# Kernel optimization log

Hardware: AMD Instinct MI355X
Metric: run time of the kernel (lower is better)

## Reference

```python
import jax, jax.numpy as jnp
import numpy as np
import math

B, T, E, HS = 8, 2048, 1024, 64  # batch, seq, n_embd, head_size (n_embd // n_head)


def setup_inputs() -> dict:
    key = jax.random.key(0)
    ks = jax.random.split(key, 7)
    sc = 1.0 / math.sqrt(E)  # roughly nn.Linear init scale
    return {
        "inputs": jax.random.normal(ks[0], (B, T, E), dtype=jnp.float32),
        "Wq": jax.random.normal(ks[1], (HS, E), dtype=jnp.float32) * sc,
        "bq": jax.random.normal(ks[2], (HS,), dtype=jnp.float32) * sc,
        "Wk": jax.random.normal(ks[3], (HS, E), dtype=jnp.float32) * sc,
        "bk": jax.random.normal(ks[4], (HS,), dtype=jnp.float32) * sc,
        "Wv": jax.random.normal(ks[5], (HS, E), dtype=jnp.float32) * sc,
        "bv": jax.random.normal(ks[6], (HS,), dtype=jnp.float32) * sc,
    }


def reference(inputs, Wq, bq, Wk, bk, Wv, bv):
    # Linear projections: x @ W.T + b  -> [B, T, HS]
    q = jnp.einsum("bte,he->bth", inputs, Wq) + bq
    k = jnp.einsum("bte,he->bth", inputs, Wk) + bk
    v = jnp.einsum("bte,he->bth", inputs, Wv) + bv

    # Scaled scores: [B, T, T]
    scores = jnp.einsum("bqh,bkh->bqk", q, k) / math.sqrt(HS)

    # Causal mask exactly as original: scores * tril - 1e12 * (1 - tril)
    tril = jnp.tril(jnp.ones((T, T), dtype=scores.dtype))
    scores = scores * tril - 1e12 * (1.0 - tril)

    attn = jax.nn.softmax(scores, axis=-1)
    # dropout p=0 (eval) -> identity
    out = jnp.einsum("bqk,bkh->bqh", attn, v)  # [B, T, HS]
    return out
```

## Files before the change

kernel.cpp:

```cpp
#include <hip/hip_runtime.h>
#include <hip/hip_bf16.h>


typedef __attribute__((ext_vector_type(8))) short short8;
typedef __attribute__((ext_vector_type(4))) float f32x4;

#if __has_builtin(__builtin_amdgcn_exp2f)
#define EXP2(x) __builtin_amdgcn_exp2f(x)
#else
#define EXP2(x) exp2f(x)
#endif

#define QSCALE 0.18033688f

__device__ inline unsigned short f2bf(float f) {
    unsigned int u = __builtin_bit_cast(unsigned int, f);
    u += 0x7FFF + ((u >> 16) & 1);
    return (unsigned short)(u >> 16);
}

__global__ __launch_bounds__(64) void prep_w(
    const float* __restrict__ Wq, const float* __restrict__ Wk,
    const float* __restrict__ Wv, unsigned short* __restrict__ Wfrag)
{
    const int ct = blockIdx.x >> 5;
    const int kk = blockIdx.x & 31;
    const int L  = threadIdx.x;
    const int l16 = L & 15, quad = L >> 4;
    const int col = ct * 16 + l16;

    const float* W; int row; float scale = 1.0f;
    if (col < 64)       { W = Wq; row = col;       scale = QSCALE; }
    else if (col < 128) { W = Wk; row = col - 64; }
    else                { W = Wv; row = col - 128; }

    const float* p = W + (size_t)row * 1024 + kk * 32 + quad * 8;
    alignas(16) unsigned short tmp[8];
    #pragma unroll
    for (int j = 0; j < 8; j++) tmp[j] = f2bf(p[j] * scale);
    unsigned short* dst = Wfrag + ((size_t)blockIdx.x * 64 + L) * 8;
    *reinterpret_cast<int4*>(dst) = *reinterpret_cast<const int4*>(tmp);
}

#define XLD 1032
__global__ __launch_bounds__(256, 4) void qkv_kernel(
    const float* __restrict__ x, const unsigned short* __restrict__ Wfrag,
    const float* __restrict__ bq, const float* __restrict__ bk,
    const float* __restrict__ bv,
    unsigned short* __restrict__ Qb, unsigned short* __restrict__ Kf,
    unsigned short* __restrict__ Vf)
{
    __shared__ alignas(16) unsigned short xs[32][XLD];

    const int tid  = threadIdx.x;
    const int m0   = blockIdx.x * 32;
    const int lane = tid & 63;
    const int w    = tid >> 6;
    const int l16  = lane & 15, quad = lane >> 4;

    #pragma unroll
    for (int i = 0; i < 16; i++) {
        int ch  = tid + 256 * i;
        int r   = ch >> 7;
        int c16 = ch & 127;
        const float* p = x + (size_t)(m0 + r) * 1024 + c16 * 8;
        float4 v0 = *reinterpret_cast<const float4*>(p);
        float4 v1 = *reinterpret_cast<const float4*>(p + 4);
        alignas(16) unsigned short t8[8] = {
            f2bf(v0.x), f2bf(v0.y), f2bf(v0.z), f2bf(v0.w),
            f2bf(v1.x), f2bf(v1.y), f2bf(v1.z), f2bf(v1.w)};
        *reinterpret_cast<int4*>(&xs[r][c16 * 8]) =
            *reinterpret_cast<const int4*>(t8);
    }
    __syncthreads();

    const int ct0 = w * 3;
    f32x4 acc[2][3];
    #pragma unroll
    for (int a = 0; a < 2; a++)
        #pragma unroll
        for (int c = 0; c < 3; c++) acc[a][c] = (f32x4){0.f, 0.f, 0.f, 0.f};

    short8 bcur[3];
    #pragma unroll
    for (int ci = 0; ci < 3; ci++)
        bcur[ci] = *reinterpret_cast<const short8*>(
            Wfrag + ((size_t)((ct0 + ci) * 32) * 64 + lane) * 8);

    for (int kk = 0; kk < 32; kk++) {
        const int kkn = (kk < 31) ? kk + 1 : 31;
        short8 bnxt[3];
        #pragma unroll
        for (int ci = 0; ci < 3; ci++)
            bnxt[ci] = *reinterpret_cast<const short8*>(
                Wfrag + ((size_t)((ct0 + ci) * 32 + kkn) * 64 + lane) * 8);

        short8 a0 = *reinterpret_cast<const short8*>(&xs[l16][kk * 32 + quad * 8]);
        short8 a1 = *reinterpret_cast<const short8*>(&xs[16 + l16][kk * 32 + quad * 8]);
        #pragma unroll
        for (int ci = 0; ci < 3; ci++) {
            acc[0][ci] = __builtin_amdgcn_mfma_f32_16x16x32_bf16(a0, bcur[ci], acc[0][ci], 0, 0, 0);
            acc[1][ci] = __builtin_amdgcn_mfma_f32_16x16x32_bf16(a1, bcur[ci], acc[1][ci], 0, 0, 0);
        }
        #pragma unroll
        for (int ci = 0; ci < 3; ci++) bcur[ci] = bnxt[ci];
    }

    const int bi = m0 >> 11;
    #pragma unroll
    for (int rt = 0; rt < 2; rt++) {
        #pragma unroll
        for (int ci = 0; ci < 3; ci++) {
            const int ct = ct0 + ci;
            const int h  = (ct & 3) * 16 + l16;
            if (ct < 4) {
                float bias = bq[h] * QSCALE;
                #pragma unroll
                for (int i = 0; i < 4; i++) {
                    size_t m = (size_t)(m0 + rt * 16 + quad * 4 + i);
                    Qb[m * 64 + h] = f2bf(acc[rt][ci][i] + bias);
                }
            } else if (ct < 8) {
                float bias = bk[h];
                #pragma unroll
                for (int i = 0; i < 4; i++) {
                    int t   = m0 + rt * 16 + quad * 4 + i;
                    int tin = t & 63;
                    int kt  = (t & 2047) >> 6;
                    int f   = ((h >> 5) << 2) | (tin >> 4);
                    int lp  = (tin & 15) | (((h >> 3) & 3) << 4);
                    Kf[(((size_t)(bi * 32 + kt) * 8 + f) * 64 + lp) * 8 + (h & 7)]
                        = f2bf(acc[rt][ci][i] + bias);
                }
            } else {
                float bias = bv[h];
                int tb  = m0 + rt * 16 + quad * 4;
                int tin = tb & 63;
                int kt  = (tb & 2047) >> 6;
                int f   = ((tin >> 5) << 2) | (h >> 4);
                int lp  = (h & 15) | (((tin >> 3) & 3) << 4);
                alignas(8) unsigned short tmp[4];
                #pragma unroll
                for (int i = 0; i < 4; i++) tmp[i] = f2bf(acc[rt][ci][i] + bias);
                unsigned short* dst =
                    Vf + (((size_t)(bi * 32 + kt) * 8 + f) * 64 + lp) * 8 + (tin & 7);
                *reinterpret_cast<int2*>(dst) = *reinterpret_cast<const int2*>(tmp);
            }
        }
    }
}

__global__ __launch_bounds__(256, 3) void attn_part(
    const unsigned short* __restrict__ Qb,
    const unsigned short* __restrict__ Kf,
    const unsigned short* __restrict__ Vf,
    float* __restrict__ Opart, float* __restrict__ Lpart)
{
    __shared__ alignas(16) unsigned short ps[4][16][72];

    const int bid = blockIdx.x;
    const int b   = bid & 7;
    const int j64 = (bid >> 3) & 31;
    const int c   = bid >> 8;
    const int nkt = j64 + 1;
    const int kt0 = c * 8;
    if (kt0 >= nkt) return;
    const int kt1 = (kt0 + 8 < nkt) ? kt0 + 8 : nkt;

    const int tid  = threadIdx.x;
    const int w    = tid >> 6;
    const int lane = tid & 63;
    const int l16  = lane & 15, quad = lane >> 4;
    const int j16  = j64 * 4 + w;
    const int q0   = j16 * 16;

    const unsigned short* qrow = Qb + ((size_t)(b * 2048 + q0 + l16)) * 64 + quad * 8;
    short8 aq0 = *reinterpret_cast<const short8*>(qrow);
    short8 aq1 = *reinterpret_cast<const short8*>(qrow + 32);

    const unsigned short* Kbat = Kf + (size_t)(b * 32) * 4096;
    const unsigned short* Vbat = Vf + (size_t)(b * 32) * 4096;

    f32x4 o[4];
    float rs[4] = {0.f, 0.f, 0.f, 0.f};
    #pragma unroll
    for (int i = 0; i < 4; i++) o[i] = (f32x4){0, 0, 0, 0};

    short8 kfr[8];
    {
        const unsigned short* kb = Kbat + (size_t)kt0 * 4096 + lane * 8;
        #pragma unroll
        for (int f = 0; f < 8; f++)
            kfr[f] = *reinterpret_cast<const short8*>(kb + f * 512);
    }

    for (int kt = kt0; kt < kt1; kt++) {
        const int ktn = (kt + 1 < kt1) ? kt + 1 : kt;
        short8 kn[8];
        {
            const unsigned short* kb = Kbat + (size_t)ktn * 4096 + lane * 8;
            #pragma unroll
            for (int f = 0; f < 8; f++)
                kn[f] = *reinterpret_cast<const short8*>(kb + f * 512);
        }
        short8 vfr[8];
        {
            const unsigned short* vb = Vbat + (size_t)kt * 4096 + lane * 8;
            #pragma unroll
            for (int f = 0; f < 8; f++)
                vfr[f] = *reinterpret_cast<const short8*>(vb + f * 512);
        }

        f32x4 s[4];
        #pragma unroll
        for (int ct = 0; ct < 4; ct++) s[ct] = (f32x4){0, 0, 0, 0};
        #pragma unroll
        for (int ks2 = 0; ks2 < 2; ks2++) {
            short8 aqf = ks2 ? aq1 : aq0;
            #pragma unroll
            for (int ct = 0; ct < 4; ct++)
                s[ct] = __builtin_amdgcn_mfma_f32_16x16x32_bf16(
                    aqf, kfr[ks2 * 4 + ct], s[ct], 0, 0, 0);
        }

        if (kt == nkt - 1) {
            #pragma unroll
            for (int ct = 0; ct < 4; ct++) {
                int col = kt * 64 + ct * 16 + l16;
                #pragma unroll
                for (int i = 0; i < 4; i++) {
                    int row = q0 + quad * 4 + i;
                    if (col > row) s[ct][i] = -1e30f;
                }
            }
        }

        #pragma unroll
        for (int ct = 0; ct < 4; ct++) {
            #pragma unroll
            for (int i = 0; i < 4; i++) {
                float p = EXP2(s[ct][i]);
                rs[i] += p;
                ps[w][quad * 4 + i][ct * 16 + l16] = f2bf(p);
            }
        }

        short8 ap0 = *reinterpret_cast<const short8*>(&ps[w][l16][quad * 8]);
        short8 ap1 = *reinterpret_cast<const short8*>(&ps[w][l16][32 + quad * 8]);

        #pragma unroll
        for (int ks2 = 0; ks2 < 2; ks2++) {
            short8 apf = ks2 ? ap1 : ap0;
            #pragma unroll
            for (int ct = 0; ct < 4; ct++)
                o[ct] = __builtin_amdgcn_mfma_f32_16x16x32_bf16(
                    apf, vfr[ks2 * 4 + ct], o[ct], 0, 0, 0);
        }

        #pragma unroll
        for (int f = 0; f < 8; f++) kfr[f] = kn[f];
    }

    const int pid = (c << 10) | (j16 << 3) | b;
    float* op = Opart + (size_t)pid * 1024;
    #pragma unroll
    for (int i = 0; i < 4; i++) {
        int r = quad * 4 + i;
        #pragma unroll
        for (int ct = 0; ct < 4; ct++)
            op[(size_t)r * 64 + ct * 16 + l16] = o[ct][i];
        float v = rs[i];
        v += __shfl_xor(v, 1);
        v += __shfl_xor(v, 2);
        v += __shfl_xor(v, 4);
        v += __shfl_xor(v, 8);
        if (l16 == 0) Lpart[(size_t)pid * 16 + r] = v;
    }
}

__global__ __launch_bounds__(256) void attn_combine(
    const float* __restrict__ Opart, const float* __restrict__ Lpart,
    float* __restrict__ out)
{
    const int t0 = blockIdx.x * 256 + threadIdx.x;
    #pragma unroll
    for (int it = 0; it < 2; it++) {
        const int v    = t0 + it * 131072;
        const int flat = v * 4;
        const int b    = flat >> 17;
        const int rem  = flat & 131071;
        const int t    = rem >> 6;
        const int h0   = rem & 63;
        const int j16  = t >> 4, row = t & 15;
        const int nch  = ((j16 >> 2) + 8) >> 3;
        const int pidb = (j16 << 3) | b;

        float4 acc = {0.f, 0.f, 0.f, 0.f};
        float  l   = 0.f;
        for (int c = 0; c < nch; c++) {
            const int pid = (c << 10) | pidb;
            const float* op = Opart + (size_t)pid * 1024 + row * 64 + h0;
            float4 x4 = *reinterpret_cast<const float4*>(op);
            acc.x += x4.x; acc.y += x4.y; acc.z += x4.z; acc.w += x4.w;
            l += Lpart[(size_t)pid * 16 + row];
        }
        const float inv = 1.f / l;
        float4 r = {acc.x * inv, acc.y * inv, acc.z * inv, acc.w * inv};
        *reinterpret_cast<float4*>(out + flat) = r;
    }
}

extern "C" void kernel_launch(void* const* d_in, const int* in_sizes, int n_in,
                              void* d_out, int out_size, void* d_ws, size_t ws_size,
                              hipStream_t stream) {
    const float* x  = (const float*)d_in[0];
    const float* Wq = (const float*)d_in[1];
    const float* bq = (const float*)d_in[2];
    const float* Wk = (const float*)d_in[3];
    const float* bk = (const float*)d_in[4];
    const float* Wv = (const float*)d_in[5];
    const float* bv = (const float*)d_in[6];
    float* out = (float*)d_out;

    unsigned short* Qb    = (unsigned short*)d_ws;
    unsigned short* Kf    = Qb + (size_t)16384 * 64;
    unsigned short* Vf    = Kf + (size_t)16384 * 64;
    unsigned short* Wfrag = Vf + (size_t)16384 * 64;
    float* Opart = (float*)(Wfrag + (size_t)12 * 32 * 64 * 8);
    float* Lpart = Opart + (size_t)4096 * 1024;

    prep_w<<<384, 64, 0, stream>>>(Wq, Wk, Wv, Wfrag);
    qkv_kernel<<<512, 256, 0, stream>>>(x, Wfrag, bq, bk, bv, Qb, Kf, Vf);
    attn_part<<<1024, 256, 0, stream>>>(Qb, Kf, Vf, Opart, Lpart);
    attn_combine<<<512, 256, 0, stream>>>(Opart, Lpart, out);
}
```

Before: 138.7 us.

## Halve attention KV chunk size, transpose score MFMA, drop K prefetch

```diff
diff --git a/kernel.cpp b/kernel.cpp
--- a/kernel.cpp
+++ b/kernel.cpp
@@ -150,7 +150,7 @@
     }
 }
 
-__global__ __launch_bounds__(256, 3) void attn_part(
+__global__ __launch_bounds__(256, 4) void attn_part(
     const unsigned short* __restrict__ Qb,
     const unsigned short* __restrict__ Kf,
     const unsigned short* __restrict__ Vf,
@@ -163,9 +163,9 @@
     const int j64 = (bid >> 3) & 31;
     const int c   = bid >> 8;
     const int nkt = j64 + 1;
-    const int kt0 = c * 8;
+    const int kt0 = c * 4;
     if (kt0 >= nkt) return;
-    const int kt1 = (kt0 + 8 < nkt) ? kt0 + 8 : nkt;
+    const int kt1 = (kt0 + 4 < nkt) ? kt0 + 4 : nkt;
 
     const int tid  = threadIdx.x;
     const int w    = tid >> 6;
@@ -182,33 +182,20 @@
     const unsigned short* Vbat = Vf + (size_t)(b * 32) * 4096;
 
     f32x4 o[4];
-    float rs[4] = {0.f, 0.f, 0.f, 0.f};
+    float rs = 0.f;
     #pragma unroll
     for (int i = 0; i < 4; i++) o[i] = (f32x4){0, 0, 0, 0};
 
-    short8 kfr[8];
-    {
-        const unsigned short* kb = Kbat + (size_t)kt0 * 4096 + lane * 8;
-        #pragma unroll
-        for (int f = 0; f < 8; f++)
-            kfr[f] = *reinterpret_cast<const short8*>(kb + f * 512);
-    }
-
     for (int kt = kt0; kt < kt1; kt++) {
-        const int ktn = (kt + 1 < kt1) ? kt + 1 : kt;
-        short8 kn[8];
+        short8 kfr[8], vfr[8];
         {
-            const unsigned short* kb = Kbat + (size_t)ktn * 4096 + lane * 8;
-            #pragma unroll
-            for (int f = 0; f < 8; f++)
-                kn[f] = *reinterpret_cast<const short8*>(kb + f * 512);
-        }
-        short8 vfr[8];
-        {
+            const unsigned short* kb = Kbat + (size_t)kt * 4096 + lane * 8;
             const unsigned short* vb = Vbat + (size_t)kt * 4096 + lane * 8;
             #pragma unroll
-            for (int f = 0; f < 8; f++)
+            for (int f = 0; f < 8; f++) {
+                kfr[f] = *reinterpret_cast<const short8*>(kb + f * 512);
                 vfr[f] = *reinterpret_cast<const short8*>(vb + f * 512);
+            }
         }
 
         f32x4 s[4];
@@ -220,29 +207,32 @@
             #pragma unroll
             for (int ct = 0; ct < 4; ct++)
                 s[ct] = __builtin_amdgcn_mfma_f32_16x16x32_bf16(
-                    aqf, kfr[ks2 * 4 + ct], s[ct], 0, 0, 0);
+                    kfr[ks2 * 4 + ct], aqf, s[ct], 0, 0, 0);
         }
 
         if (kt == nkt - 1) {
+            const int qr = q0 + l16;
             #pragma unroll
             for (int ct = 0; ct < 4; ct++) {
-                int col = kt * 64 + ct * 16 + l16;
                 #pragma unroll
                 for (int i = 0; i < 4; i++) {
-                    int row = q0 + quad * 4 + i;
-                    if (col > row) s[ct][i] = -1e30f;
+                    int kc = kt * 64 + ct * 16 + quad * 4 + i;
+                    if (kc > qr) s[ct][i] = -1e30f;
                 }
             }
         }
 
         #pragma unroll
         for (int ct = 0; ct < 4; ct++) {
+            alignas(8) unsigned short t4[4];
             #pragma unroll
             for (int i = 0; i < 4; i++) {
                 float p = EXP2(s[ct][i]);
-                rs[i] += p;
-                ps[w][quad * 4 + i][ct * 16 + l16] = f2bf(p);
+                rs += p;
+                t4[i] = f2bf(p);
             }
+            *reinterpret_cast<int2*>(&ps[w][l16][ct * 16 + quad * 4]) =
+                *reinterpret_cast<const int2*>(t4);
         }
 
         short8 ap0 = *reinterpret_cast<const short8*>(&ps[w][l16][quad * 8]);
@@ -256,9 +246,6 @@
                 o[ct] = __builtin_amdgcn_mfma_f32_16x16x32_bf16(
                     apf, vfr[ks2 * 4 + ct], o[ct], 0, 0, 0);
         }
-
-        #pragma unroll
-        for (int f = 0; f < 8; f++) kfr[f] = kn[f];
     }
 
     const int pid = (c << 10) | (j16 << 3) | b;
@@ -269,13 +256,11 @@
         #pragma unroll
         for (int ct = 0; ct < 4; ct++)
             op[(size_t)r * 64 + ct * 16 + l16] = o[ct][i];
-        float v = rs[i];
-        v += __shfl_xor(v, 1);
-        v += __shfl_xor(v, 2);
-        v += __shfl_xor(v, 4);
-        v += __shfl_xor(v, 8);
-        if (l16 == 0) Lpart[(size_t)pid * 16 + r] = v;
-    }
+    }
+    float v = rs;
+    v += __shfl_xor(v, 16);
+    v += __shfl_xor(v, 32);
+    if (quad == 0) Lpart[(size_t)pid * 16 + l16] = v;
 }
 
 __global__ __launch_bounds__(256) void attn_combine(
@@ -292,7 +277,7 @@
         const int t    = rem >> 6;
         const int h0   = rem & 63;
         const int j16  = t >> 4, row = t & 15;
-        const int nch  = ((j16 >> 2) + 8) >> 3;
+        const int nch  = ((j16 >> 2) + 4) >> 2;
         const int pidb = (j16 << 3) | b;
 
         float4 acc = {0.f, 0.f, 0.f, 0.f};
@@ -327,10 +312,10 @@
     unsigned short* Vf    = Kf + (size_t)16384 * 64;
     unsigned short* Wfrag = Vf + (size_t)16384 * 64;
     float* Opart = (float*)(Wfrag + (size_t)12 * 32 * 64 * 8);
-    float* Lpart = Opart + (size_t)4096 * 1024;
+    float* Lpart = Opart + (size_t)8192 * 1024;
 
     prep_w<<<384, 64, 0, stream>>>(Wq, Wk, Wv, Wfrag);
     qkv_kernel<<<512, 256, 0, stream>>>(x, Wfrag, bq, bk, bv, Qb, Kf, Vf);
-    attn_part<<<1024, 256, 0, stream>>>(Qb, Kf, Vf, Opart, Lpart);
+    attn_part<<<2048, 256, 0, stream>>>(Qb, Kf, Vf, Opart, Lpart);
     attn_combine<<<512, 256, 0, stream>>>(Opart, Lpart, out);
 }
```

New measurement: 135.8 us. 2.1% less time.
